# Performance work log

Hardware: AMD Instinct MI355X
Metric: run time of the kernel (lower is better)

## Reference

```python
import jax, jax.numpy as jnp
import numpy as np

BS, N, XC, K, YS = 64, 1024, 1024, 256, 768

def setup_inputs() -> dict:
    key = jax.random.key(0)
    ks = jax.random.split(key, 5)
    return {
        "x": jax.random.normal(ks[0], (BS, N, XC), dtype=jnp.float32),
        "y": jax.random.normal(ks[1], (BS, YS), dtype=jnp.float32),
        "W_ch": jax.random.normal(ks[2], (K, XC), dtype=jnp.float32) * 0.02,
        "b_ch": jax.random.normal(ks[3], (K,), dtype=jnp.float32) * 0.02,
        "W_y": jax.random.normal(ks[4], (K, YS), dtype=jnp.float32) * 0.02,
    }

def reference(x, y, W_ch, b_ch, W_y):
    # y_k: [bs, k] (no bias)
    y_k = jnp.einsum('bs,ks->bk', y, W_y)
    # channel affine on every spatial position, batched: [bs, n, k]
    x_k = jnp.einsum('bnc,kc->bnk', x, W_ch) + b_ch
    # add per-sample y_k (broadcast over spatial dim), tanh, softmax over k
    z = jnp.tanh(x_k + y_k[:, None, :])
    attn = jax.nn.softmax(z, axis=-1)
    # torch.cat over dim=0 of per-sample [n, k] blocks -> [bs*n, k]
    return attn.reshape(-1, attn.shape[-1])
```

## Files before the change

### kernel.cpp

```cpp
#include <hip/hip_runtime.h>


#define XC    1024
#define KOUT  256
#define NT    16
#define ABSZ  16384
#define LDSZ  49152

typedef float        f32x4_t  __attribute__((ext_vector_type(4)));
typedef unsigned int u32x4_t  __attribute__((ext_vector_type(4)));
typedef unsigned int u32x2_t  __attribute__((ext_vector_type(2)));
typedef __bf16       bf16x8_t __attribute__((ext_vector_type(8)));

__device__ __forceinline__ unsigned short f2bf(float f) {
  unsigned int u = __float_as_uint(f);
  u += 0x7fffu + ((u >> 16) & 1u);
  return (unsigned short)(u >> 16);
}

__device__ __forceinline__ float fast_tanh(float v) {
  float e = __expf(2.0f * v);
  return 1.0f - 2.0f / (e + 1.0f);
}

__device__ __forceinline__ void async_copy16(const void* lds, const void* g) {
  __builtin_amdgcn_global_load_lds(
      (const __attribute__((address_space(1))) void*)g,
      (__attribute__((address_space(3))) void*)lds, 16, 0, 0);
}

#define PIPE_WAIT(N) asm volatile("s_waitcnt vmcnt(" #N ")" ::: "memory")

__global__ void prep_kernel(const float* __restrict__ Wch,
                            const float* __restrict__ y,
                            const float* __restrict__ Wy,
                            const float* __restrict__ bch,
                            unsigned short* __restrict__ wbf,
                            float* __restrict__ biasws) {
  if (blockIdx.x < 256) {
    const int k = blockIdx.x;
    const int u = threadIdx.x;
    f32x4_t v = ((const f32x4_t*)(Wch + k * XC))[u];
    const int c0   = u << 2;
    const int t    = c0 >> 6;
    const int ch   = (c0 & 63) >> 3;
    const int kk   = ch >> 2;
    const int lg   = ch & 3;
    const int half = (c0 >> 2) & 1;
    const int wv   = k >> 6;
    const int ni   = (k >> 4) & 3;
    const int lr   = k & 15;
    const int lane = (lg << 4) | lr;
    unsigned int lo = (unsigned int)f2bf(v.x) | ((unsigned int)f2bf(v.y) << 16);
    unsigned int hi = (unsigned int)f2bf(v.z) | ((unsigned int)f2bf(v.w) << 16);
    char* p = (char*)wbf +
              ((size_t)((((t << 2) + wv) * 2 + kk) * 4 + ni) << 10) +
              (lane << 4) + (half << 3);
    *(u32x2_t*)p = (u32x2_t){lo, hi};
  } else {
    __shared__ __align__(16) float ys[768];
    const int b = blockIdx.x - 256;
    const int k = threadIdx.x;
    for (int i = k; i < 768; i += 256) ys[i] = y[b * 768 + i];
    __syncthreads();
    const f32x4_t* w4 = (const f32x4_t*)(Wy + k * 768);
    const f32x4_t* y4 = (const f32x4_t*)ys;
    float s = 0.f;
#pragma unroll 8
    for (int i = 0; i < 192; ++i) {
      f32x4_t w = w4[i], a = y4[i];
      s = fmaf(w.x, a.x, s); s = fmaf(w.y, a.y, s);
      s = fmaf(w.z, a.z, s); s = fmaf(w.w, a.w, s);
    }
    biasws[b * 256 + k] = s + bch[k];
  }
}

__global__ __launch_bounds__(256, 3) void fused_kernel(
    const float* __restrict__ x, const unsigned short* __restrict__ wbf,
    const float* __restrict__ bias, float* __restrict__ out) {
  __shared__ __align__(16) unsigned char smem[LDSZ];
  const int tid = threadIdx.x;
  const int l   = tid & 63;
  const int w   = tid >> 6;
  const int lr  = l & 15;
  const int lg  = l >> 4;
  const int m0  = blockIdx.x << 6;
  const int bidx = m0 >> 10;

  f32x4_t acc[4][4];
#pragma unroll
  for (int i = 0; i < 4; ++i)
#pragma unroll
    for (int j = 0; j < 4; ++j) acc[i][j] = (f32x4_t){0.f, 0.f, 0.f, 0.f};

  const char* xbase = (const char*)x + ((size_t)m0 << 12);
  const char* wsrc  = (const char*)wbf + (w << 13) + (l << 4);
  bf16x8_t bfrA[8], bfrB[8];

#define DMA_A(tt, buf) do {                                                  \
    _Pragma("unroll")                                                        \
    for (int i = 0; i < 4; ++i) {                                            \
      const int row = (w << 4) + (i << 2) + (l >> 4);                        \
      const int sw  = ((l >> 1) & 7) ^ (row & 7);                            \
      const char* g = xbase + ((size_t)row << 12) + ((tt) << 8) +            \
                      (sw << 5) + ((l & 1) << 4);                            \
      async_copy16(smem + (buf) * ABSZ + (w << 12) + (i << 10), g);          \
    }                                                                        \
  } while (0)

#define LOADB(dst, tt) do {                                                  \
    const char* g = wsrc + (size_t)(tt) * 32768;                             \
    _Pragma("unroll")                                                        \
    for (int f = 0; f < 8; ++f)                                              \
      dst[f] = __builtin_bit_cast(bf16x8_t, *(const u32x4_t*)(g + (f << 10)));\
  } while (0)

#define COMPUTE(bufc, bsrc) do {                                             \
    const f32x4_t* aB = (const f32x4_t*)(smem + (bufc) * ABSZ);              \
    _Pragma("unroll")                                                        \
    for (int kk = 0; kk < 2; ++kk) {                                         \
      bf16x8_t afr[4];                                                       \
      _Pragma("unroll")                                                      \
      for (int mi = 0; mi < 4; ++mi) {                                       \
        const int row = (mi << 4) + lr;                                      \
        const int sw  = (((kk << 2) | lg) ^ (row & 7));                      \
        f32x4_t lo = aB[(row << 4) + (sw << 1)];                             \
        f32x4_t hi = aB[(row << 4) + (sw << 1) + 1];                         \
        bf16x8_t t_;                                                         \
        t_[0] = (__bf16)lo.x; t_[1] = (__bf16)lo.y;                          \
        t_[2] = (__bf16)lo.z; t_[3] = (__bf16)lo.w;                          \
        t_[4] = (__bf16)hi.x; t_[5] = (__bf16)hi.y;                          \
        t_[6] = (__bf16)hi.z; t_[7] = (__bf16)hi.w;                          \
        afr[mi] = t_;                                                        \
      }                                                                      \
      _Pragma("unroll")                                                      \
      for (int mi = 0; mi < 4; ++mi)                                         \
        _Pragma("unroll")                                                    \
        for (int nj = 0; nj < 4; ++nj)                                       \
          acc[mi][nj] = __builtin_amdgcn_mfma_f32_16x16x32_bf16(             \
              afr[mi], bsrc[(kk << 2) | nj], acc[mi][nj], 0, 0, 0);          \
    }                                                                        \
  } while (0)

  DMA_A(0, 0);
  LOADB(bfrA, 0);
  DMA_A(1, 1);

#pragma unroll
  for (int s = 0; s < NT; ++s) {
    if (s < NT - 1) { PIPE_WAIT(4); } else { PIPE_WAIT(0); }
    __builtin_amdgcn_sched_barrier(0);
    __builtin_amdgcn_s_barrier();
    __builtin_amdgcn_sched_barrier(0);
    if (s + 1 < NT) {
      if (s & 1) LOADB(bfrA, s + 1); else LOADB(bfrB, s + 1);
    }
    if (s + 2 < NT) DMA_A(s + 2, (s + 2) % 3);
    if (s & 1) COMPUTE(s % 3, bfrB); else COMPUTE(s % 3, bfrA);
  }
  __syncthreads();

#undef DMA_A
#undef LOADB
#undef COMPUTE

  float* wred    = (float*)smem;
  float* rowstat = (float*)(smem + 1024);

  float brow[4];
#pragma unroll
  for (int ni = 0; ni < 4; ++ni)
    brow[ni] = bias[(bidx << 8) + (w << 6) + (ni << 4) + lr];

#pragma unroll
  for (int mi = 0; mi < 4; ++mi)
#pragma unroll
    for (int ni = 0; ni < 4; ++ni)
#pragma unroll
      for (int r = 0; r < 4; ++r)
        acc[mi][ni][r] = fast_tanh(acc[mi][ni][r] + brow[ni]);

#pragma unroll
  for (int mi = 0; mi < 4; ++mi)
#pragma unroll
    for (int r = 0; r < 4; ++r) {
      float m = fmaxf(fmaxf(acc[mi][0][r], acc[mi][1][r]),
                      fmaxf(acc[mi][2][r], acc[mi][3][r]));
      m = fmaxf(m, __shfl_xor(m, 1));
      m = fmaxf(m, __shfl_xor(m, 2));
      m = fmaxf(m, __shfl_xor(m, 4));
      m = fmaxf(m, __shfl_xor(m, 8));
      if (lr == 0) wred[(w << 6) + (mi << 4) + (lg << 2) + r] = m;
    }
  __syncthreads();
  if (tid < 64)
    rowstat[tid] = fmaxf(fmaxf(wred[tid], wred[64 + tid]),
                         fmaxf(wred[128 + tid], wred[192 + tid]));
  __syncthreads();

#pragma unroll
  for (int mi = 0; mi < 4; ++mi)
#pragma unroll
    for (int r = 0; r < 4; ++r) {
      const int row = (mi << 4) + (lg << 2) + r;
      const float m = rowstat[row];
      float s = 0.f;
#pragma unroll
      for (int ni = 0; ni < 4; ++ni) {
        float e = __expf(acc[mi][ni][r] - m);
        acc[mi][ni][r] = e;
        s += e;
      }
      s += __shfl_xor(s, 1);
      s += __shfl_xor(s, 2);
      s += __shfl_xor(s, 4);
      s += __shfl_xor(s, 8);
      if (lr == 0) wred[(w << 6) + row] = s;
    }
  __syncthreads();
  if (tid < 64)
    rowstat[tid] = 1.0f / (wred[tid] + wred[64 + tid] +
                           wred[128 + tid] + wred[192 + tid]);
  __syncthreads();

#pragma unroll
  for (int mi = 0; mi < 4; ++mi)
#pragma unroll
    for (int r = 0; r < 4; ++r) {
      const int row = (mi << 4) + (lg << 2) + r;
      const float rinv = rowstat[row];
      float* orow = out + (size_t)(m0 + row) * KOUT + (w << 6) + lr;
#pragma unroll
      for (int ni = 0; ni < 4; ++ni)
        orow[ni << 4] = acc[mi][ni][r] * rinv;
    }
}

extern "C" void kernel_launch(void* const* d_in, const int* in_sizes, int n_in,
                              void* d_out, int out_size, void* d_ws, size_t ws_size,
                              hipStream_t stream) {
  (void)in_sizes; (void)n_in; (void)out_size; (void)ws_size;
  const float* x   = (const float*)d_in[0];
  const float* y   = (const float*)d_in[1];
  const float* Wch = (const float*)d_in[2];
  const float* bch = (const float*)d_in[3];
  const float* Wy  = (const float*)d_in[4];
  float* out = (float*)d_out;
  unsigned short* wbf = (unsigned short*)d_ws;
  float* biasws = (float*)((char*)d_ws + 512 * 1024);

  hipLaunchKernelGGL(prep_kernel, dim3(320), dim3(256), 0, stream,
                     Wch, y, Wy, bch, wbf, biasws);
  hipLaunchKernelGGL(fused_kernel, dim3(1024), dim3(256), 0, stream,
                     x, wbf, biasws, out);
}
```

Baseline: 130.8 us.

## Restructure GEMM so each wave owns full rows, streaming A from registers and B via LDS

The work split changes from waves sharing a 64x256 tile (A staged in LDS, B per-wave in registers) to each wave owning 16 full rows. Each wave loads its A fragments straight from global memory into registers, while the bf16 weight tiles are DMA'd into double-buffered LDS and shared by all waves. Because each wave now holds whole rows, the softmax reduction uses only intra-wave shuffles, which removes the LDS reductions and the block barriers. It also rotates the K-tile start per block (t0) to spread memory traffic, and uses a cheaper bf16 packing with round-half-up instead of round-to-even. In exchange, LDS grows to 64KB and occupancy drops from 3 to 2 blocks per CU.

```diff
diff --git a/kernel.cpp b/kernel.cpp
--- a/kernel.cpp
+++ b/kernel.cpp
@@ -3,9 +3,7 @@
 
 #define XC    1024
 #define KOUT  256
-#define NT    16
-#define ABSZ  16384
-#define LDSZ  49152
+#define LDSZ  65536
 
 typedef float        f32x4_t  __attribute__((ext_vector_type(4)));
 typedef unsigned int u32x4_t  __attribute__((ext_vector_type(4)));
@@ -18,18 +16,25 @@
   return (unsigned short)(u >> 16);
 }
 
+__device__ __forceinline__ unsigned int pack2bf(float a, float b) {
+  unsigned int ua = __float_as_uint(a) + 0x8000u;
+  unsigned int ub = __float_as_uint(b) + 0x8000u;
+  return (ua >> 16) | (ub & 0xffff0000u);
+}
+
 __device__ __forceinline__ float fast_tanh(float v) {
   float e = __expf(2.0f * v);
   return 1.0f - 2.0f / (e + 1.0f);
 }
 
-__device__ __forceinline__ void async_copy16(const void* lds, const void* g) {
+__device__ __forceinline__ void async_copy16(void* lds, const void* g) {
   __builtin_amdgcn_global_load_lds(
       (const __attribute__((address_space(1))) void*)g,
       (__attribute__((address_space(3))) void*)lds, 16, 0, 0);
 }
 
-#define PIPE_WAIT(N) asm volatile("s_waitcnt vmcnt(" #N ")" ::: "memory")
+#define PIPE_WAIT_(N) asm volatile("s_waitcnt vmcnt(" #N ")" ::: "memory")
+#define PIPE_WAIT(N)  PIPE_WAIT_(N)
 
 __global__ void prep_kernel(const float* __restrict__ Wch,
                             const float* __restrict__ y,
@@ -76,7 +81,7 @@
   }
 }
 
-__global__ __launch_bounds__(256, 3) void fused_kernel(
+__global__ __launch_bounds__(256, 2) void fused_kernel(
     const float* __restrict__ x, const unsigned short* __restrict__ wbf,
     const float* __restrict__ bias, float* __restrict__ out) {
   __shared__ __align__(16) unsigned char smem[LDSZ];
@@ -87,154 +92,141 @@
   const int lg  = l >> 4;
   const int m0  = blockIdx.x << 6;
   const int bidx = m0 >> 10;
-
-  f32x4_t acc[4][4];
-#pragma unroll
-  for (int i = 0; i < 4; ++i)
-#pragma unroll
-    for (int j = 0; j < 4; ++j) acc[i][j] = (f32x4_t){0.f, 0.f, 0.f, 0.f};
-
-  const char* xbase = (const char*)x + ((size_t)m0 << 12);
-  const char* wsrc  = (const char*)wbf + (w << 13) + (l << 4);
-  bf16x8_t bfrA[8], bfrB[8];
-
-#define DMA_A(tt, buf) do {                                                  \
+  const int t0  = blockIdx.x & 15;
+
+  f32x4_t acc[16];
+#pragma unroll
+  for (int i = 0; i < 16; ++i) acc[i] = (f32x4_t){0.f, 0.f, 0.f, 0.f};
+
+  const char* xrow = (const char*)x +
+      ((size_t)(m0 + (w << 4) + lr) << 12) + (lg << 5);
+  const char* wsrc = (const char*)wbf;
+  f32x4_t av0[2], av1[2], av2[2], av3[2];
+
+#define LOADA(dst, s_) do {                                                  \
+    const int off_ = (((((s_) >> 1) + t0) & 15) << 8) + (((s_) & 1) << 7);   \
+    dst[0] = *(const f32x4_t*)(xrow + off_);                                 \
+    dst[1] = *(const f32x4_t*)(xrow + off_ + 16);                            \
+  } while (0)
+
+#define DMAB(T_) do {                                                        \
+    const int tile_ = ((T_) + t0) & 15;                                      \
+    const char* g_ = wsrc + ((size_t)tile_ << 15) + (w << 13) + (l << 4);    \
+    unsigned char* d_ = smem + (((T_) & 1) << 15) + (w << 13);               \
     _Pragma("unroll")                                                        \
-    for (int i = 0; i < 4; ++i) {                                            \
-      const int row = (w << 4) + (i << 2) + (l >> 4);                        \
-      const int sw  = ((l >> 1) & 7) ^ (row & 7);                            \
-      const char* g = xbase + ((size_t)row << 12) + ((tt) << 8) +            \
-                      (sw << 5) + ((l & 1) << 4);                            \
-      async_copy16(smem + (buf) * ABSZ + (w << 12) + (i << 10), g);          \
+    for (int i_ = 0; i_ < 8; ++i_)                                           \
+      async_copy16(d_ + (i_ << 10), g_ + (i_ << 10));                        \
+  } while (0)
+
+#define PACK(avC)                                                            \
+    u32x4_t afu_;                                                            \
+    afu_[0] = pack2bf(avC[0].x, avC[0].y);                                   \
+    afu_[1] = pack2bf(avC[0].z, avC[0].w);                                   \
+    afu_[2] = pack2bf(avC[1].x, avC[1].y);                                   \
+    afu_[3] = pack2bf(avC[1].z, avC[1].w);                                   \
+    bf16x8_t afr_ = __builtin_bit_cast(bf16x8_t, afu_);
+
+#define MFMAS(bufL, kkL) do {                                                \
+    const u32x4_t* bB_ = (const u32x4_t*)(smem + ((bufL) << 15));            \
+    _Pragma("unroll")                                                        \
+    for (int wv2 = 0; wv2 < 4; ++wv2) {                                      \
+      bf16x8_t bfr_[4];                                                      \
+      _Pragma("unroll")                                                      \
+      for (int ni = 0; ni < 4; ++ni)                                         \
+        bfr_[ni] = __builtin_bit_cast(bf16x8_t,                              \
+            bB_[(((((wv2 << 1) | (kkL)) << 2) | ni) << 6) + l]);             \
+      _Pragma("unroll")                                                      \
+      for (int ni = 0; ni < 4; ++ni)                                         \
+        acc[(wv2 << 2) | ni] = __builtin_amdgcn_mfma_f32_16x16x32_bf16(      \
+            afr_, bfr_[ni], acc[(wv2 << 2) | ni], 0, 0, 0);                  \
     }                                                                        \
   } while (0)
 
-#define LOADB(dst, tt) do {                                                  \
-    const char* g = wsrc + (size_t)(tt) * 32768;                             \
-    _Pragma("unroll")                                                        \
-    for (int f = 0; f < 8; ++f)                                              \
-      dst[f] = __builtin_bit_cast(bf16x8_t, *(const u32x4_t*)(g + (f << 10)));\
-  } while (0)
-
-#define COMPUTE(bufc, bsrc) do {                                             \
-    const f32x4_t* aB = (const f32x4_t*)(smem + (bufc) * ABSZ);              \
-    _Pragma("unroll")                                                        \
-    for (int kk = 0; kk < 2; ++kk) {                                         \
-      bf16x8_t afr[4];                                                       \
-      _Pragma("unroll")                                                      \
-      for (int mi = 0; mi < 4; ++mi) {                                       \
-        const int row = (mi << 4) + lr;                                      \
-        const int sw  = (((kk << 2) | lg) ^ (row & 7));                      \
-        f32x4_t lo = aB[(row << 4) + (sw << 1)];                             \
-        f32x4_t hi = aB[(row << 4) + (sw << 1) + 1];                         \
-        bf16x8_t t_;                                                         \
-        t_[0] = (__bf16)lo.x; t_[1] = (__bf16)lo.y;                          \
-        t_[2] = (__bf16)lo.z; t_[3] = (__bf16)lo.w;                          \
-        t_[4] = (__bf16)hi.x; t_[5] = (__bf16)hi.y;                          \
-        t_[6] = (__bf16)hi.z; t_[7] = (__bf16)hi.w;                          \
-        afr[mi] = t_;                                                        \
-      }                                                                      \
-      _Pragma("unroll")                                                      \
-      for (int mi = 0; mi < 4; ++mi)                                         \
-        _Pragma("unroll")                                                    \
-        for (int nj = 0; nj < 4; ++nj)                                       \
-          acc[mi][nj] = __builtin_amdgcn_mfma_f32_16x16x32_bf16(             \
-              afr[mi], bsrc[(kk << 2) | nj], acc[mi][nj], 0, 0, 0);          \
-    }                                                                        \
-  } while (0)
-
-  DMA_A(0, 0);
-  LOADB(bfrA, 0);
-  DMA_A(1, 1);
-
-#pragma unroll
-  for (int s = 0; s < NT; ++s) {
-    if (s < NT - 1) { PIPE_WAIT(4); } else { PIPE_WAIT(0); }
-    __builtin_amdgcn_sched_barrier(0);
-    __builtin_amdgcn_s_barrier();
-    __builtin_amdgcn_sched_barrier(0);
-    if (s + 1 < NT) {
-      if (s & 1) LOADB(bfrA, s + 1); else LOADB(bfrB, s + 1);
+#define BARRIER(VM) do {                                                     \
+    PIPE_WAIT(VM);                                                           \
+    __builtin_amdgcn_s_barrier();                                            \
+    __builtin_amdgcn_sched_barrier(0);                                       \
+  } while (0)
+
+#define STEPE(T_, avC, DODMA, DOLA) {                                        \
+    if (DODMA) DMAB((T_) + 1);                                               \
+    PACK(avC);                                                               \
+    if (DOLA) LOADA(avC, 2 * (T_) + 4);                                      \
+    MFMAS((T_) & 1, 0);                                                      \
+  }
+#define STEPO(T_, avC, DOLA, DOBAR, VM) {                                    \
+    PACK(avC);                                                               \
+    if (DOLA) LOADA(avC, 2 * (T_) + 5);                                      \
+    MFMAS((T_) & 1, 1);                                                      \
+    if (DOBAR) BARRIER(VM);                                                  \
+  }
+
+  DMAB(0);
+  LOADA(av0, 0); LOADA(av1, 1); LOADA(av2, 2); LOADA(av3, 3);
+  BARRIER(8);
+
+  STEPE( 0, av0, 1, 1)  STEPO( 0, av1, 1, 1, 4)
+  STEPE( 1, av2, 1, 1)  STEPO( 1, av3, 1, 1, 4)
+  STEPE( 2, av0, 1, 1)  STEPO( 2, av1, 1, 1, 4)
+  STEPE( 3, av2, 1, 1)  STEPO( 3, av3, 1, 1, 4)
+  STEPE( 4, av0, 1, 1)  STEPO( 4, av1, 1, 1, 4)
+  STEPE( 5, av2, 1, 1)  STEPO( 5, av3, 1, 1, 4)
+  STEPE( 6, av0, 1, 1)  STEPO( 6, av1, 1, 1, 4)
+  STEPE( 7, av2, 1, 1)  STEPO( 7, av3, 1, 1, 4)
+  STEPE( 8, av0, 1, 1)  STEPO( 8, av1, 1, 1, 4)
+  STEPE( 9, av2, 1, 1)  STEPO( 9, av3, 1, 1, 4)
+  STEPE(10, av0, 1, 1)  STEPO(10, av1, 1, 1, 4)
+  STEPE(11, av2, 1, 1)  STEPO(11, av3, 1, 1, 4)
+  STEPE(12, av0, 1, 1)  STEPO(12, av1, 1, 1, 4)
+  STEPE(13, av2, 1, 1)  STEPO(13, av3, 1, 1, 4)
+  STEPE(14, av0, 1, 0)  STEPO(14, av1, 0, 1, 0)
+  STEPE(15, av2, 0, 0)  STEPO(15, av3, 0, 0, 0)
+
+#undef LOADA
+#undef DMAB
+#undef PACK
+#undef MFMAS
+#undef BARRIER
+#undef STEPE
+#undef STEPO
+
+  float brow[16];
+#pragma unroll
+  for (int c = 0; c < 16; ++c)
+    brow[c] = bias[(bidx << 8) + (c << 4) + lr];
+
+#pragma unroll
+  for (int c = 0; c < 16; ++c)
+#pragma unroll
+    for (int r = 0; r < 4; ++r)
+      acc[c][r] = fast_tanh(acc[c][r] + brow[c]);
+
+#pragma unroll
+  for (int r = 0; r < 4; ++r) {
+    float m = acc[0][r];
+#pragma unroll
+    for (int c = 1; c < 16; ++c) m = fmaxf(m, acc[c][r]);
+    m = fmaxf(m, __shfl_xor(m, 1));
+    m = fmaxf(m, __shfl_xor(m, 2));
+    m = fmaxf(m, __shfl_xor(m, 4));
+    m = fmaxf(m, __shfl_xor(m, 8));
+    float ssum = 0.f;
+#pragma unroll
+    for (int c = 0; c < 16; ++c) {
+      float e = __expf(acc[c][r] - m);
+      acc[c][r] = e;
+      ssum += e;
     }
-    if (s + 2 < NT) DMA_A(s + 2, (s + 2) % 3);
-    if (s & 1) COMPUTE(s % 3, bfrB); else COMPUTE(s % 3, bfrA);
-  }
-  __syncthreads();
-
-#undef DMA_A
-#undef LOADB
-#undef COMPUTE
-
-  float* wred    = (float*)smem;
-  float* rowstat = (float*)(smem + 1024);
-
-  float brow[4];
-#pragma unroll
-  for (int ni = 0; ni < 4; ++ni)
-    brow[ni] = bias[(bidx << 8) + (w << 6) + (ni << 4) + lr];
-
-#pragma unroll
-  for (int mi = 0; mi < 4; ++mi)
-#pragma unroll
-    for (int ni = 0; ni < 4; ++ni)
-#pragma unroll
-      for (int r = 0; r < 4; ++r)
-        acc[mi][ni][r] = fast_tanh(acc[mi][ni][r] + brow[ni]);
-
-#pragma unroll
-  for (int mi = 0; mi < 4; ++mi)
-#pragma unroll
-    for (int r = 0; r < 4; ++r) {
-      float m = fmaxf(fmaxf(acc[mi][0][r], acc[mi][1][r]),
-                      fmaxf(acc[mi][2][r], acc[mi][3][r]));
-      m = fmaxf(m, __shfl_xor(m, 1));
-      m = fmaxf(m, __shfl_xor(m, 2));
-      m = fmaxf(m, __shfl_xor(m, 4));
-      m = fmaxf(m, __shfl_xor(m, 8));
-      if (lr == 0) wred[(w << 6) + (mi << 4) + (lg << 2) + r] = m;
-    }
-  __syncthreads();
-  if (tid < 64)
-    rowstat[tid] = fmaxf(fmaxf(wred[tid], wred[64 + tid]),
-                         fmaxf(wred[128 + tid], wred[192 + tid]));
-  __syncthreads();
-
-#pragma unroll
-  for (int mi = 0; mi < 4; ++mi)
-#pragma unroll
-    for (int r = 0; r < 4; ++r) {
-      const int row = (mi << 4) + (lg << 2) + r;
-      const float m = rowstat[row];
-      float s = 0.f;
-#pragma unroll
-      for (int ni = 0; ni < 4; ++ni) {
-        float e = __expf(acc[mi][ni][r] - m);
-        acc[mi][ni][r] = e;
-        s += e;
-      }
-      s += __shfl_xor(s, 1);
-      s += __shfl_xor(s, 2);
-      s += __shfl_xor(s, 4);
-      s += __shfl_xor(s, 8);
-      if (lr == 0) wred[(w << 6) + row] = s;
-    }
-  __syncthreads();
-  if (tid < 64)
-    rowstat[tid] = 1.0f / (wred[tid] + wred[64 + tid] +
-                           wred[128 + tid] + wred[192 + tid]);
-  __syncthreads();
-
-#pragma unroll
-  for (int mi = 0; mi < 4; ++mi)
-#pragma unroll
-    for (int r = 0; r < 4; ++r) {
-      const int row = (mi << 4) + (lg << 2) + r;
-      const float rinv = rowstat[row];
-      float* orow = out + (size_t)(m0 + row) * KOUT + (w << 6) + lr;
-#pragma unroll
-      for (int ni = 0; ni < 4; ++ni)
-        orow[ni << 4] = acc[mi][ni][r] * rinv;
-    }
+    ssum += __shfl_xor(ssum, 1);
+    ssum += __shfl_xor(ssum, 2);
+    ssum += __shfl_xor(ssum, 4);
+    ssum += __shfl_xor(ssum, 8);
+    const float rinv = 1.0f / ssum;
+    float* orow = out + ((size_t)(m0 + (w << 4) + (lg << 2) + r) << 8) + lr;
+#pragma unroll
+    for (int c = 0; c < 16; ++c)
+      orow[c << 4] = acc[c][r] * rinv;
+  }
 }
 
 extern "C" void kernel_launch(void* const* d_in, const int* in_sizes, int n_in,
```

New measurement: 118.1 us. -9.7%, faster.
